# Performance work log

Measured on AMD Instinct MI355X. Metric: run time of the kernel, lower is better.

Reference implementation:

```python
import jax, jax.numpy as jnp
import numpy as np

HEADS = 4
DIM_HEAD = 32


def setup_inputs() -> dict:
    key = jax.random.key(0)
    k1, k2, k3 = jax.random.split(key, 3)
    b, c, h, w = 2, 256, 64, 64
    hidden = HEADS * DIM_HEAD  # 128
    x = jax.random.normal(k1, (b, c, h, w), dtype=jnp.float32)
    # conv1x1 weights (out_ch, in_ch); scaled like torch default init
    w_qkv = jax.random.normal(k2, (hidden * 3, c), dtype=jnp.float32) * (1.0 / np.sqrt(c))
    w_out = jax.random.normal(k3, (c, hidden), dtype=jnp.float32) * (1.0 / np.sqrt(hidden))
    b_out = jnp.zeros((c,), dtype=jnp.float32)
    return {"x": x, "w_qkv": w_qkv, "w_out": w_out, "b_out": b_out}


def reference(x, w_qkv, w_out, b_out):
    b, c, h, w = x.shape
    hw = h * w
    scale = DIM_HEAD ** -0.5
    # 1x1 conv == channel GEMM
    qkv = jnp.einsum('oc,bchw->bohw', w_qkv, x)
    # replicate torch view(b, heads, dim_head, 3, h*w): q/k/v interleaved per channel
    qkv = qkv.reshape(b, HEADS, DIM_HEAD, 3, hw)
    q = qkv[..., 0, :] * scale           # (b, H, d, N)
    k = qkv[..., 1, :]
    v = qkv[..., 2, :]
    sim = jnp.einsum('bhdi,bhdj->bhij', q, k)   # (b, H, N, N)
    attn = jax.nn.softmax(sim, axis=-1)         # max-subtract softmax (same math)
    out = jnp.einsum('bhij,bhdj->bhid', attn, v)  # (b, H, N, d)
    out = out.transpose(0, 1, 3, 2).reshape(b, HEADS * DIM_HEAD, h, w)
    return jnp.einsum('oc,bchw->bohw', w_out, out) + b_out[None, :, None, None]
```

## Files before the change

### kernel.cpp

```cpp
#include <hip/hip_runtime.h>

#define HEADS 4
#define DIM_HEAD 32
#define NB 2
#define NC 256
#define HW 4096
#define HIDDEN 128
#define NBH (NB*HEADS)
#define ROWS_TOTAL (NBH*HW)

typedef _Float16 f16;
typedef _Float16 f16x8 __attribute__((ext_vector_type(8)));
typedef __fp16 fp16x2 __attribute__((ext_vector_type(2)));
typedef float f32x4 __attribute__((ext_vector_type(4)));

#define XT_OFF   0u
#define QT_OFF   (4u<<20)
#define KT_OFF   (6u<<20)
#define VH_OFF   (8u<<20)
#define HIDT_OFF (10u<<20)
#define WQH_OFF  (12u<<20)
#define WOH_OFF  ((12u<<20) + (256u<<10))
#define PART_OFF (13u<<20)
#define NSPLIT 4

__device__ __forceinline__ f16x8 ldg_f16x8(const f16* p) {
    union { uint4 u; f16x8 v; } t;
    t.u = *reinterpret_cast<const uint4*>(p);
    return t.v;
}
__device__ __forceinline__ unsigned packh2(float a, float b) {
    union { fp16x2 h; unsigned u; } t;
    t.h = __builtin_amdgcn_cvt_pkrtz(a, b);
    return t.u;
}

__global__ __launch_bounds__(256) void prep(const float* __restrict__ x,
                                            const float* __restrict__ wqkv,
                                            const float* __restrict__ wout,
                                            f16* __restrict__ xt,
                                            f16* __restrict__ wqh,
                                            f16* __restrict__ woh) {
    __shared__ float T[64][65];
    if (blockIdx.x < 512) {
        const int idx = blockIdx.x;
        const int b = idx >> 8, rem = idx & 255;
        const int c0 = (rem >> 6) * 64, s0 = (rem & 63) * 64;
        const int t = threadIdx.x;
        #pragma unroll
        for (int i = 0; i < 16; ++i) {
            int e = t + i * 256;
            int c = e >> 6, s = e & 63;
            T[c][s] = x[((size_t)(b * NC + c0 + c)) * HW + s0 + s];
        }
        __syncthreads();
        const int s = t >> 2, cg = (t & 3) * 16;
        unsigned ov[8];
        #pragma unroll
        for (int i = 0; i < 8; ++i)
            ov[i] = packh2(T[cg + 2 * i][s], T[cg + 2 * i + 1][s]);
        const int srow = s0 + s;
        f16* dst = xt + ((((size_t)(b * 256 + (srow >> 4))) * 8 + ((c0 + cg) >> 5)) << 9)
                      + (srow & 15) * 32 + (cg & 31);
        *reinterpret_cast<uint4*>(dst)     = make_uint4(ov[0], ov[1], ov[2], ov[3]);
        *reinterpret_cast<uint4*>(dst + 8) = make_uint4(ov[4], ov[5], ov[6], ov[7]);
        return;
    }
    const int tid = (blockIdx.x - 512) * 256 + threadIdx.x;
    const float QSCALE = 0.17677669529663687f * 1.4426950408889634f;
    if (tid < 24576) {
        int o_lin = tid >> 6;
        int c4 = (tid & 63) * 4;
        int which = o_lin >> 7, r = o_lin & 127;
        int head = r >> 5, d = r & 31;
        int o_g = head * 96 + d * 3 + which;
        float4 v = *reinterpret_cast<const float4*>(wqkv + o_g * 256 + c4);
        float scl = (which == 0) ? QSCALE : 1.0f;
        uint2 pv;
        pv.x = packh2(v.x * scl, v.y * scl);
        pv.y = packh2(v.z * scl, v.w * scl);
        f16* dst = wqh + (((o_lin >> 4) * 8 + (c4 >> 5)) << 9)
                       + (o_lin & 15) * 32 + (c4 & 31);
        *reinterpret_cast<uint2*>(dst) = pv;
    } else if (tid < 24576 + 8192) {
        int t2 = tid - 24576;
        int o = t2 >> 5;
        int c4 = (t2 * 4) & 127;
        float4 v = *reinterpret_cast<const float4*>(wout + t2 * 4);
        uint2 pv;
        pv.x = packh2(v.x, v.y);
        pv.y = packh2(v.z, v.w);
        f16* dst = woh + (((o >> 4) * 4 + (c4 >> 5)) << 9)
                       + (o & 15) * 32 + (c4 & 31);
        *reinterpret_cast<uint2*>(dst) = pv;
    }
}

__global__ __launch_bounds__(256) void qkv_mfma(const f16* __restrict__ xt,
                                                const f16* __restrict__ wqh,
                                                f16* __restrict__ qt,
                                                f16* __restrict__ kt,
                                                f16* __restrict__ vh) {
    const int w = threadIdx.x >> 6, lane = threadIdx.x & 63;
    const int q15 = lane & 15, quad = lane >> 4;
    const int b = blockIdx.z;
    const int sTile = blockIdx.x * 64 + (w & 1) * 32;
    const int oTile = blockIdx.y * 64 + (w >> 1) * 32;
    const f16* At = xt + (((size_t)(b * 256 + (sTile >> 4))) << 12);
    const f16* Bt = wqh + (((size_t)(oTile >> 4)) << 12);
    const int fo = q15 * 32 + quad * 8;

    f32x4 acc[2][2];
    #pragma unroll
    for (int i = 0; i < 2; ++i)
        #pragma unroll
        for (int j = 0; j < 2; ++j) acc[i][j] = (f32x4){0.f, 0.f, 0.f, 0.f};

    #pragma unroll
    for (int kc = 0; kc < 256; kc += 32) {
        const int kt5 = (kc >> 5) << 9;
        f16x8 a0 = ldg_f16x8(At + kt5 + fo);
        f16x8 a1 = ldg_f16x8(At + 4096 + kt5 + fo);
        f16x8 b0 = ldg_f16x8(Bt + kt5 + fo);
        f16x8 b1 = ldg_f16x8(Bt + 4096 + kt5 + fo);
        acc[0][0] = __builtin_amdgcn_mfma_f32_16x16x32_f16(a0, b0, acc[0][0], 0, 0, 0);
        acc[0][1] = __builtin_amdgcn_mfma_f32_16x16x32_f16(a0, b1, acc[0][1], 0, 0, 0);
        acc[1][0] = __builtin_amdgcn_mfma_f32_16x16x32_f16(a1, b0, acc[1][0], 0, 0, 0);
        acc[1][1] = __builtin_amdgcn_mfma_f32_16x16x32_f16(a1, b1, acc[1][1], 0, 0, 0);
    }

    #pragma unroll
    for (int si = 0; si < 2; ++si)
        #pragma unroll
        for (int oj = 0; oj < 2; ++oj) {
            int o_lin = oTile + oj * 16 + q15;
            int which = o_lin >> 7;
            int r = o_lin & 127;
            int head = r >> 5, d = r & 31;
            int bh = b * HEADS + head;
            int s2 = sTile + si * 16 + quad * 4;
            if (which == 2) {
                uint2 pv;
                pv.x = packh2(acc[si][oj][0], acc[si][oj][1]);
                pv.y = packh2(acc[si][oj][2], acc[si][oj][3]);
                f16* dst = vh + ((((size_t)bh * 128 + (sTile >> 5)) * 32 + d) << 5)
                              + quad * 8 + si * 4;
                *reinterpret_cast<uint2*>(dst) = pv;
            } else {
                f16* dst = (which == 0 ? qt : kt) + (size_t)bh * HW * 32;
                #pragma unroll
                for (int r2 = 0; r2 < 4; ++r2)
                    dst[(size_t)(s2 + r2) * 32 + d] = (f16)acc[si][oj][r2];
            }
        }
}

#define MFMA16(A,B,C) __builtin_amdgcn_mfma_f32_16x16x32_f16(A,B,C,0,0,0)

#define LDKV(kd0,kd1,vd0,vd1,J)                                             \
    kd0 = ldg_f16x8(Kb + (size_t)((J) + q15) * 32 + quad * 8);              \
    kd1 = ldg_f16x8(Kb + (size_t)((J) + 16 + q15) * 32 + quad * 8);         \
    vd0 = ldg_f16x8(Vb + (((size_t)((J) >> 5) * 32 + q15) << 5) + quad * 8);\
    vd1 = ldg_f16x8(Vb + (((size_t)((J) >> 5) * 32 + 16 + q15) << 5) + quad * 8);

#define CHUNK(kf0_,kf1_,vf0_,vf1_)                                       \
    {                                                                    \
        const f32x4 z = {0.f, 0.f, 0.f, 0.f};                            \
        f32x4 s0a = MFMA16(kf0_, qf0, z);                                \
        f32x4 s1a = MFMA16(kf1_, qf0, z);                                \
        f32x4 s0b = MFMA16(kf0_, qf1, z);                                \
        f32x4 s1b = MFMA16(kf1_, qf1, z);                                \
        float ea[8], eb[8];                                              \
        _Pragma("unroll")                                                \
        for (int r = 0; r < 4; ++r) {                                    \
            ea[r]   = __builtin_amdgcn_exp2f(s0a[r]);                    \
            ea[4+r] = __builtin_amdgcn_exp2f(s1a[r]);                    \
            eb[r]   = __builtin_amdgcn_exp2f(s0b[r]);                    \
            eb[4+r] = __builtin_amdgcn_exp2f(s1b[r]);                    \
        }                                                                \
        l0 += (ea[0]+ea[1])+(ea[2]+ea[3])+(ea[4]+ea[5])+(ea[6]+ea[7]);   \
        l1 += (eb[0]+eb[1])+(eb[2]+eb[3])+(eb[4]+eb[5])+(eb[6]+eb[7]);   \
        union { unsigned u[4]; f16x8 v; } pa, pb;                        \
        pa.u[0] = packh2(ea[0], ea[1]); pa.u[1] = packh2(ea[2], ea[3]);  \
        pa.u[2] = packh2(ea[4], ea[5]); pa.u[3] = packh2(ea[6], ea[7]);  \
        pb.u[0] = packh2(eb[0], eb[1]); pb.u[1] = packh2(eb[2], eb[3]);  \
        pb.u[2] = packh2(eb[4], eb[5]); pb.u[3] = packh2(eb[6], eb[7]);  \
        acc[0][0] = MFMA16(vf0_, pa.v, acc[0][0]);                       \
        acc[0][1] = MFMA16(vf1_, pa.v, acc[0][1]);                       \
        acc[1][0] = MFMA16(vf0_, pb.v, acc[1][0]);                       \
        acc[1][1] = MFMA16(vf1_, pb.v, acc[1][1]);                       \
    }

__global__ __launch_bounds__(256) void attn_mfma(const f16* __restrict__ qt,
                                                 const f16* __restrict__ kt,
                                                 const f16* __restrict__ vh,
                                                 float* __restrict__ part) {
    const int w    = threadIdx.x >> 6;
    const int lane = threadIdx.x & 63;
    const int q15  = lane & 15;
    const int quad = lane >> 4;

    const int L    = blockIdx.x;
    const int xcd  = L & 7;
    const int slot = L >> 3;
    const int combo = xcd * 4 + (slot >> 5);
    const int qblk  = slot & 31;
    const int bh    = combo & 7;
    const int split = combo >> 3;
    const int qbase = (qblk * 4 + w) * 32;

    const f16* Qb = qt + (size_t)bh * HW * 32;
    const f16* Kb = kt + (size_t)bh * HW * 32;
    const f16* Vb = vh + (size_t)bh * 128 * 1024;

    f16x8 qf0 = ldg_f16x8(Qb + (size_t)(qbase + q15) * 32 + quad * 8);
    f16x8 qf1 = ldg_f16x8(Qb + (size_t)(qbase + 16 + q15) * 32 + quad * 8);

    f32x4 acc[2][2];
    #pragma unroll
    for (int a = 0; a < 2; ++a)
        #pragma unroll
        for (int b2 = 0; b2 < 2; ++b2)
            acc[a][b2] = (f32x4){0.f, 0.f, 0.f, 0.f};
    float l0 = 0.f, l1 = 0.f;

    const int j0   = split * 1024;
    const int span = min(1024, HW - j0);

    f16x8 ka0, ka1, va0, va1, kb0, kb1, vb0, vb1;
    LDKV(ka0, ka1, va0, va1, j0);
    LDKV(kb0, kb1, vb0, vb1, j0 + 32);

    for (int jc = 0; jc < span; jc += 64) {
        CHUNK(ka0, ka1, va0, va1);
        LDKV(ka0, ka1, va0, va1, j0 + jc + 64);
        CHUNK(kb0, kb1, vb0, vb1);
        LDKV(kb0, kb1, vb0, vb1, j0 + jc + 96);
    }

    float* P = part + (size_t)split * 33 * ROWS_TOTAL;
    #pragma unroll
    for (int qb = 0; qb < 2; ++qb) {
        float lv = qb ? l1 : l0;
        lv += __shfl_xor(lv, 16, 64);
        lv += __shfl_xor(lv, 32, 64);
        const int grow = bh * HW + qbase + qb * 16 + q15;
        if (quad == 0) P[grow] = lv;
        #pragma unroll
        for (int t = 0; t < 2; ++t)
            #pragma unroll
            for (int r = 0; r < 4; ++r) {
                int d = t * 16 + quad * 4 + r;
                P[(size_t)(1 + d) * ROWS_TOTAL + grow] = acc[qb][t][r];
            }
    }
}

__global__ __launch_bounds__(256) void attn_merge(const float* __restrict__ part,
                                                  f16* __restrict__ hidt) {
    const int grow = blockIdx.x * 64 + (threadIdx.x & 63);
    const int dq   = threadIdx.x >> 6;
    float l = 0.f;
    #pragma unroll
    for (int sp = 0; sp < NSPLIT; ++sp)
        l += part[(size_t)sp * 33 * ROWS_TOTAL + grow];
    const float inv = 1.0f / l;
    const int bh = grow >> 12, s = grow & 4095;
    const int b = bh >> 2, h = bh & 3;

    unsigned ov[4];
    #pragma unroll
    for (int i = 0; i < 4; ++i) {
        const int d2 = dq * 4 + i;
        float o0 = 0.f, o1 = 0.f;
        #pragma unroll
        for (int sp = 0; sp < NSPLIT; ++sp) {
            const float* P = part + (size_t)sp * 33 * ROWS_TOTAL + grow;
            o0 += P[(size_t)(1 + 2 * d2) * ROWS_TOTAL];
            o1 += P[(size_t)(2 + 2 * d2) * ROWS_TOTAL];
        }
        ov[i] = packh2(o0 * inv, o1 * inv);
    }
    f16* dst = hidt + ((((size_t)(b * 256 + (s >> 4))) * 4 + h) << 9)
                    + (s & 15) * 32 + dq * 8;
    *reinterpret_cast<uint4*>(dst) = make_uint4(ov[0], ov[1], ov[2], ov[3]);
}

__global__ __launch_bounds__(256) void outp_mfma(const f16* __restrict__ hidt,
                                                 const f16* __restrict__ woh,
                                                 const float* __restrict__ bout,
                                                 float* __restrict__ out) {
    const int w = threadIdx.x >> 6, lane = threadIdx.x & 63;
    const int q15 = lane & 15, quad = lane >> 4;
    const int b = blockIdx.z;
    const int sTile = blockIdx.x * 64 + (w & 1) * 32;
    const int oTile = blockIdx.y * 64 + (w >> 1) * 32;
    const f16* At = hidt + (((size_t)(b * 256 + (sTile >> 4))) << 11);
    const f16* Bt = woh + (((size_t)(oTile >> 4)) << 11);
    const int fo = q15 * 32 + quad * 8;

    f32x4 acc[2][2];
    #pragma unroll
    for (int i = 0; i < 2; ++i)
        #pragma unroll
        for (int j = 0; j < 2; ++j) acc[i][j] = (f32x4){0.f, 0.f, 0.f, 0.f};

    #pragma unroll
    for (int kc = 0; kc < 128; kc += 32) {
        const int kt5 = (kc >> 5) << 9;
        f16x8 a0 = ldg_f16x8(At + kt5 + fo);
        f16x8 a1 = ldg_f16x8(At + 2048 + kt5 + fo);
        f16x8 b0 = ldg_f16x8(Bt + kt5 + fo);
        f16x8 b1 = ldg_f16x8(Bt + 2048 + kt5 + fo);
        acc[0][0] = __builtin_amdgcn_mfma_f32_16x16x32_f16(a0, b0, acc[0][0], 0, 0, 0);
        acc[0][1] = __builtin_amdgcn_mfma_f32_16x16x32_f16(a0, b1, acc[0][1], 0, 0, 0);
        acc[1][0] = __builtin_amdgcn_mfma_f32_16x16x32_f16(a1, b0, acc[1][0], 0, 0, 0);
        acc[1][1] = __builtin_amdgcn_mfma_f32_16x16x32_f16(a1, b1, acc[1][1], 0, 0, 0);
    }

    #pragma unroll
    for (int oj = 0; oj < 2; ++oj) {
        const int o = oTile + oj * 16 + q15;
        const float bias = bout[o];
        #pragma unroll
        for (int si = 0; si < 2; ++si) {
            const int s2 = sTile + si * 16 + quad * 4;
            float4 v = make_float4(acc[si][oj][0] + bias, acc[si][oj][1] + bias,
                                   acc[si][oj][2] + bias, acc[si][oj][3] + bias);
            *reinterpret_cast<float4*>(out + ((size_t)(b * NC + o)) * HW + s2) = v;
        }
    }
}

extern "C" void kernel_launch(void* const* d_in, const int* in_sizes, int n_in,
                              void* d_out, int out_size, void* d_ws, size_t ws_size,
                              hipStream_t stream) {
    const float* x    = (const float*)d_in[0];
    const float* wqkv = (const float*)d_in[1];
    const float* wout = (const float*)d_in[2];
    const float* bout = (const float*)d_in[3];
    float* out = (float*)d_out;
    char* wsb  = (char*)d_ws;

    f16*   XT   = (f16*)(wsb + XT_OFF);
    f16*   QT   = (f16*)(wsb + QT_OFF);
    f16*   KT   = (f16*)(wsb + KT_OFF);
    f16*   VH   = (f16*)(wsb + VH_OFF);
    f16*   HIDT = (f16*)(wsb + HIDT_OFF);
    f16*   WQH  = (f16*)(wsb + WQH_OFF);
    f16*   WOH  = (f16*)(wsb + WOH_OFF);
    float* PART = (float*)(wsb + PART_OFF);

    prep     <<<dim3(640), 256, 0, stream>>>(x, wqkv, wout, XT, WQH, WOH);
    qkv_mfma <<<dim3(64, 6, NB), 256, 0, stream>>>(XT, WQH, QT, KT, VH);
    attn_mfma<<<dim3(1024), 256, 0, stream>>>(QT, KT, VH, PART);
    attn_merge<<<dim3(512), 256, 0, stream>>>(PART, HIDT);
    outp_mfma<<<dim3(64, 4, NB), 256, 0, stream>>>(HIDT, WOH, bout, out);
}
```

Measured before the change: 122.1 us.

## Fuse split-KV attention merge into attention kernel via shared memory

Moves the four key splits of each query block into the four waves of one workgroup, and reduces their partial sums and row sums through LDS inside the attention kernel. This removes the fp32 partial buffer round trip through global memory and the separate merge kernel launch. The trade-off is that each workgroup now covers 32 query rows instead of 128. The XCD-aware block remapping is dropped, and 16KB of LDS per block may reduce occupancy.

```diff
diff --git a/kernel.cpp b/kernel.cpp
--- a/kernel.cpp
+++ b/kernel.cpp
@@ -21,8 +21,6 @@
 #define HIDT_OFF (10u<<20)
 #define WQH_OFF  (12u<<20)
 #define WOH_OFF  ((12u<<20) + (256u<<10))
-#define PART_OFF (13u<<20)
-#define NSPLIT 4
 
 __device__ __forceinline__ f16x8 ldg_f16x8(const f16* p) {
     union { uint4 u; f16x8 v; } t;
@@ -191,23 +189,21 @@
         acc[1][1] = MFMA16(vf1_, pb.v, acc[1][1]);                       \
     }
 
-__global__ __launch_bounds__(256) void attn_mfma(const f16* __restrict__ qt,
-                                                 const f16* __restrict__ kt,
-                                                 const f16* __restrict__ vh,
-                                                 float* __restrict__ part) {
+__global__ __launch_bounds__(256) void attn_fused(const f16* __restrict__ qt,
+                                                  const f16* __restrict__ kt,
+                                                  const f16* __restrict__ vh,
+                                                  f16* __restrict__ hidt) {
+    __shared__ float Lo[4 * 4 * 256];
+    __shared__ float Ll[4][2][16];
     const int w    = threadIdx.x >> 6;
     const int lane = threadIdx.x & 63;
     const int q15  = lane & 15;
     const int quad = lane >> 4;
 
     const int L    = blockIdx.x;
-    const int xcd  = L & 7;
-    const int slot = L >> 3;
-    const int combo = xcd * 4 + (slot >> 5);
-    const int qblk  = slot & 31;
-    const int bh    = combo & 7;
-    const int split = combo >> 3;
-    const int qbase = (qblk * 4 + w) * 32;
+    const int bh   = L & 7;
+    const int qblk = L >> 3;
+    const int qbase = qblk * 32;
 
     const f16* Qb = qt + (size_t)bh * HW * 32;
     const f16* Kb = kt + (size_t)bh * HW * 32;
@@ -224,7 +220,7 @@
             acc[a][b2] = (f32x4){0.f, 0.f, 0.f, 0.f};
     float l0 = 0.f, l1 = 0.f;
 
-    const int j0   = split * 1024;
+    const int j0   = w * 1024;
     const int span = min(1024, HW - j0);
 
     f16x8 ka0, ka1, va0, va1, kb0, kb1, vb0, vb1;
@@ -238,52 +234,41 @@
         LDKV(kb0, kb1, vb0, vb1, j0 + jc + 96);
     }
 
-    float* P = part + (size_t)split * 33 * ROWS_TOTAL;
-    #pragma unroll
-    for (int qb = 0; qb < 2; ++qb) {
-        float lv = qb ? l1 : l0;
-        lv += __shfl_xor(lv, 16, 64);
-        lv += __shfl_xor(lv, 32, 64);
-        const int grow = bh * HW + qbase + qb * 16 + q15;
-        if (quad == 0) P[grow] = lv;
+    l0 += __shfl_xor(l0, 16, 64);
+    l0 += __shfl_xor(l0, 32, 64);
+    l1 += __shfl_xor(l1, 16, 64);
+    l1 += __shfl_xor(l1, 32, 64);
+    if (quad == 0) { Ll[w][0][q15] = l0; Ll[w][1][q15] = l1; }
+
+    float* Wo = Lo + w * 1024;
+    #pragma unroll
+    for (int qb = 0; qb < 2; ++qb)
         #pragma unroll
         for (int t = 0; t < 2; ++t)
-            #pragma unroll
-            for (int r = 0; r < 4; ++r) {
-                int d = t * 16 + quad * 4 + r;
-                P[(size_t)(1 + d) * ROWS_TOTAL + grow] = acc[qb][t][r];
-            }
-    }
-}
-
-__global__ __launch_bounds__(256) void attn_merge(const float* __restrict__ part,
-                                                  f16* __restrict__ hidt) {
-    const int grow = blockIdx.x * 64 + (threadIdx.x & 63);
-    const int dq   = threadIdx.x >> 6;
-    float l = 0.f;
-    #pragma unroll
-    for (int sp = 0; sp < NSPLIT; ++sp)
-        l += part[(size_t)sp * 33 * ROWS_TOTAL + grow];
+            *reinterpret_cast<f32x4*>(Wo + (qb * 2 + t) * 256 + lane * 4) = acc[qb][t];
+    __syncthreads();
+
+    const int row  = threadIdx.x >> 3;
+    const int dg   = threadIdx.x & 7;
+    const int qb   = row >> 4, q15r = row & 15;
+    const int t_   = dg >> 2, quadr = dg & 3;
+    const float l = Ll[0][qb][q15r] + Ll[1][qb][q15r] + Ll[2][qb][q15r] + Ll[3][qb][q15r];
     const float inv = 1.0f / l;
-    const int bh = grow >> 12, s = grow & 4095;
+    float o0 = 0.f, o1 = 0.f, o2 = 0.f, o3 = 0.f;
+    #pragma unroll
+    for (int ww = 0; ww < 4; ++ww) {
+        const float* p = Lo + ww * 1024 + (qb * 2 + t_) * 256 + (quadr * 16 + q15r) * 4;
+        o0 += p[0]; o1 += p[1]; o2 += p[2]; o3 += p[3];
+    }
+    uint2 pv;
+    pv.x = packh2(o0 * inv, o1 * inv);
+    pv.y = packh2(o2 * inv, o3 * inv);
+    const int s = qbase + row;
     const int b = bh >> 2, h = bh & 3;
-
-    unsigned ov[4];
-    #pragma unroll
-    for (int i = 0; i < 4; ++i) {
-        const int d2 = dq * 4 + i;
-        float o0 = 0.f, o1 = 0.f;
-        #pragma unroll
-        for (int sp = 0; sp < NSPLIT; ++sp) {
-            const float* P = part + (size_t)sp * 33 * ROWS_TOTAL + grow;
-            o0 += P[(size_t)(1 + 2 * d2) * ROWS_TOTAL];
-            o1 += P[(size_t)(2 + 2 * d2) * ROWS_TOTAL];
-        }
-        ov[i] = packh2(o0 * inv, o1 * inv);
-    }
+    const int d = t_ * 16 + quadr * 4;
     f16* dst = hidt + ((((size_t)(b * 256 + (s >> 4))) * 4 + h) << 9)
-                    + (s & 15) * 32 + dq * 8;
-    *reinterpret_cast<uint4*>(dst) = make_uint4(ov[0], ov[1], ov[2], ov[3]);
+                    + (s & 15) * 32 + d;
+    *reinterpret_cast<uint2*>(dst) = pv;
 }
 
 __global__ __launch_bounds__(256) void outp_mfma(const f16* __restrict__ hidt,
@@ -349,11 +334,9 @@
     f16*   HIDT = (f16*)(wsb + HIDT_OFF);
     f16*   WQH  = (f16*)(wsb + WQH_OFF);
     f16*   WOH  = (f16*)(wsb + WOH_OFF);
-    float* PART = (float*)(wsb + PART_OFF);
-
-    prep     <<<dim3(640), 256, 0, stream>>>(x, wqkv, wout, XT, WQH, WOH);
-    qkv_mfma <<<dim3(64, 6, NB), 256, 0, stream>>>(XT, WQH, QT, KT, VH);
-    attn_mfma<<<dim3(1024), 256, 0, stream>>>(QT, KT, VH, PART);
-    attn_merge<<<dim3(512), 256, 0, stream>>>(PART, HIDT);
-    outp_mfma<<<dim3(64, 4, NB), 256, 0, stream>>>(HIDT, WOH, bout, out);
-}
+
+    prep      <<<dim3(640), 256, 0, stream>>>(x, wqkv, wout, XT, WQH, WOH);
+    qkv_mfma  <<<dim3(64, 6, NB), 256, 0, stream>>>(XT, WQH, QT, KT, VH);
+    attn_fused<<<dim3(1024), 256, 0, stream>>>(QT, KT, VH, HIDT);
+    outp_mfma <<<dim3(64, 4, NB), 256, 0, stream>>>(HIDT, WOH, bout, out);
+}
```

After: 113.6 us. 1.07x faster.
